# Kernel optimization log

Measured on AMD Instinct MI355X. Metric: run time of the kernel, lower is better.

The kernel has to match this reference:

```python
import jax, jax.numpy as jnp
import numpy as np

N = 50000        # num nodes
D = 128          # hidden_dim
E = 800000       # num edges (avg_degree = 16)
LN_EPS = 1e-5    # torch LayerNorm default eps


def setup_inputs() -> dict:
    key = jax.random.key(0)
    ks = jax.random.split(key, 8)
    x = jax.random.normal(ks[0], (N, D), dtype=jnp.float32)
    edge_rows = jax.random.randint(ks[1], (E,), 0, N, dtype=jnp.int32)
    edge_cols = jax.random.randint(ks[2], (E,), 0, N, dtype=jnp.int32)
    # Parameters (xavier_uniform for lin1 gain=1.0, lin2 gain=0.5; zero biases)
    lim1 = float(np.sqrt(6.0 / (D + D)))           # gain 1.0
    lim2 = 0.5 * float(np.sqrt(6.0 / (D + D)))     # gain 0.5
    W1 = jax.random.uniform(ks[3], (D, D), minval=-lim1, maxval=lim1, dtype=jnp.float32)
    W2 = jax.random.uniform(ks[4], (D, D), minval=-lim2, maxval=lim2, dtype=jnp.float32)
    b1 = jnp.zeros((D,), dtype=jnp.float32)
    b2 = jnp.zeros((D,), dtype=jnp.float32)
    gamma = jnp.ones((D,), dtype=jnp.float32)      # LayerNorm weight
    beta = jnp.zeros((D,), dtype=jnp.float32)      # LayerNorm bias
    eps = jnp.zeros((), dtype=jnp.float32)         # learnable eps, init 0.0
    return {"x": x, "edge_rows": edge_rows, "edge_cols": edge_cols,
            "W1": W1, "b1": b1, "W2": W2, "b2": b2,
            "gamma": gamma, "beta": beta, "eps": eps}


def layer_norm(x, gamma, beta):
    mu = jnp.mean(x, axis=-1, keepdims=True)
    var = jnp.mean((x - mu) ** 2, axis=-1, keepdims=True)
    return (x - mu) * jax.lax.rsqrt(var + LN_EPS) * gamma + beta


def reference(x, edge_rows, edge_cols, W1, b1, W2, b2, gamma, beta, eps):
    h = layer_norm(x, gamma, beta)                               # [N, D]
    # sparse.mm(adj_t, h): neighbor_sum[i] = sum over edges (i <- j) of h[j]
    neighbor_sum = jax.ops.segment_sum(h[edge_cols], edge_rows, num_segments=N)
    h = (1.0 + eps) * h + neighbor_sum
    h = jax.nn.silu(h @ W1.T + b1)                               # lin1 + SiLU
    h = h @ W2.T + b2                                            # lin2 (dropout p=0 -> identity)
    return x + h
```

## Files before the change

kernel.cpp:

```cpp
#include <hip/hip_runtime.h>
#include <hip/hip_bf16.h>

#define N_NODES 50000
#define DIM 128
#define N_EDGES 800000
#define NBUCKETS 196
#define BINA_EPB 4096
#define NBLKA 196
#define SEGCAP 64
#define BUCKET_CAP 6144
#define LN_BLOCKS 12500

typedef __bf16 bf16_t;
typedef bf16_t bf16x2 __attribute__((ext_vector_type(2)));
typedef bf16_t bf16x4 __attribute__((ext_vector_type(4)));
typedef bf16_t bf16x8 __attribute__((ext_vector_type(8)));
typedef float f32x4 __attribute__((ext_vector_type(4)));

__device__ __forceinline__ float bf_lo(unsigned int u) {
  return __uint_as_float(u << 16);
}
__device__ __forceinline__ float bf_hi(unsigned int u) {
  return __uint_as_float(u & 0xffff0000u);
}

__global__ __launch_bounds__(256) void k_ln_binA(
    const float* __restrict__ x, const float* __restrict__ gamma,
    const float* __restrict__ beta, bf16_t* __restrict__ h,
    const int* __restrict__ erows, const int* __restrict__ ecols,
    unsigned int* __restrict__ tmp, int* __restrict__ cnt) {
  __shared__ int sh_hist[256];
  __shared__ int sh_cur[256];
  const int t = threadIdx.x;

  if (blockIdx.x < NBLKA) {
    const int blk = blockIdx.x;
    sh_hist[t] = 0;
    __syncthreads();
    const int base = blk * BINA_EPB;
    int bkt[16];
    unsigned int pk[16];
#pragma unroll
    for (int i = 0; i < 16; ++i) {
      const int e = base + i * 256 + t;
      if (e < N_EDGES) {
        const int d = erows[e];
        bkt[i] = d >> 8;
        pk[i] = ((unsigned int)(d & 255) << 16) | (unsigned int)ecols[e];
        atomicAdd(&sh_hist[bkt[i]], 1);
      } else {
        bkt[i] = -1;
      }
    }
    __syncthreads();
    if (t < NBUCKETS) cnt[t * NBLKA + blk] = min(sh_hist[t], SEGCAP);
    sh_cur[t] = 0;
    __syncthreads();
#pragma unroll
    for (int i = 0; i < 16; ++i) {
      if (bkt[i] >= 0) {
        const int pos = atomicAdd(&sh_cur[bkt[i]], 1);
        if (pos < SEGCAP)
          tmp[((size_t)bkt[i] * NBLKA + blk) * SEGCAP + pos] = pk[i];
      }
    }
    return;
  }

  const int lane = t & 63;
  const int row  = (blockIdx.x - NBLKA) * 4 + (t >> 6);
  const float2 v = *(const float2*)(x + (size_t)row * DIM + lane * 2);
  float s  = v.x + v.y;
  float ss = v.x * v.x + v.y * v.y;
#pragma unroll
  for (int d = 1; d < 64; d <<= 1) {
    s  += __shfl_xor(s, d);
    ss += __shfl_xor(ss, d);
  }
  const float mu   = s * (1.0f / 128.0f);
  const float var  = ss * (1.0f / 128.0f) - mu * mu;
  const float rstd = rsqrtf(var + 1e-5f);
  const float2 g = *(const float2*)(gamma + lane * 2);
  const float2 b = *(const float2*)(beta + lane * 2);
  const float h0 = (v.x - mu) * rstd * g.x + b.x;
  const float h1 = (v.y - mu) * rstd * g.y + b.y;
  *(bf16x2*)(h + (size_t)row * DIM + lane * 2) = (bf16x2){(bf16_t)h0, (bf16_t)h1};
}

__global__ __launch_bounds__(256) void k_binB(
    const unsigned int* __restrict__ tmp, const int* __restrict__ cnt,
    int* __restrict__ nstart, int* __restrict__ nend,
    unsigned short* __restrict__ sorted) {
  __shared__ unsigned int stage[BUCKET_CAP];
  __shared__ int sh_cnt[256];
  __shared__ int sh_cur[256];
  __shared__ int wsum[4];
  const int b = blockIdx.x, t = threadIdx.x;
  const int lane = t & 63, w = t >> 6;

  const int c = (t < NBLKA) ? cnt[b * NBLKA + t] : 0;
  int v = c;
#pragma unroll
  for (int d = 1; d < 64; d <<= 1) {
    const int n = __shfl_up(v, d);
    if (lane >= d) v += n;
  }
  if (lane == 63) wsum[w] = v;
  __syncthreads();
  int woff = 0;
  for (int k = 0; k < w; ++k) woff += wsum[k];
  const int soff = v + woff - c;
  int total = wsum[0] + wsum[1] + wsum[2] + wsum[3];
  if (total > BUCKET_CAP) total = BUCKET_CAP;

  if (c > 0) {
    const unsigned int* seg = tmp + ((size_t)b * NBLKA + t) * SEGCAP;
    for (int j = 0; j < c; ++j) {
      const int p = soff + j;
      if (p < BUCKET_CAP) stage[p] = seg[j];
    }
  }
  __syncthreads();

  sh_cnt[t] = 0;
  __syncthreads();
  for (int e = t; e < total; e += 256)
    atomicAdd(&sh_cnt[stage[e] >> 16], 1);
  __syncthreads();

  const int val = sh_cnt[t];
  int v2 = val;
#pragma unroll
  for (int d = 1; d < 64; d <<= 1) {
    const int n = __shfl_up(v2, d);
    if (lane >= d) v2 += n;
  }
  __syncthreads();
  if (lane == 63) wsum[w] = v2;
  __syncthreads();
  int woff2 = 0;
  for (int k = 0; k < w; ++k) woff2 += wsum[k];
  const int rs = b * BUCKET_CAP;
  const int st = rs + v2 + woff2 - val;
  const int nidx = b * 256 + t;
  if (nidx < N_NODES) { nstart[nidx] = st; nend[nidx] = st + val; }
  sh_cur[t] = st;
  __syncthreads();

  for (int e = t; e < total; e += 256) {
    const unsigned int pv = stage[e];
    const int pos = atomicAdd(&sh_cur[pv >> 16], 1);
    sorted[pos] = (unsigned short)(pv & 0xffffu);
  }
}

__global__ __launch_bounds__(256) void k_gather(
    const uint2* __restrict__ h4, const int* __restrict__ nstart,
    const int* __restrict__ nend, const unsigned short* __restrict__ sorted,
    const float* __restrict__ epsp, bf16_t* __restrict__ acc) {
  const int tid  = threadIdx.x;
  const int lane = tid & 63;
  const int half = lane >> 5;
  const int l31  = lane & 31;
  const int node = blockIdx.x * 4 + (tid >> 6);
  const int s = nstart[node], e = nend[node];
  f32x4 a0 = {0.f, 0.f, 0.f, 0.f};
  f32x4 a1 = {0.f, 0.f, 0.f, 0.f};
  f32x4 a2 = {0.f, 0.f, 0.f, 0.f};
  f32x4 a3 = {0.f, 0.f, 0.f, 0.f};
  for (int base = s; base < e; base += 64) {
    const int cnt = e - base;
    const int m = cnt < 64 ? cnt : 64;
    const int myidx = (lane < m) ? (int)sorted[base + lane] : 0;
    for (int j = 0; j < m; j += 8) {
      const int o0 = j + half;
      const int o1 = j + 2 + half;
      const int o2 = j + 4 + half;
      const int o3 = j + 6 + half;
      const int s0 = __shfl(myidx, o0);
      const int s1 = __shfl(myidx, o1);
      const int s2 = __shfl(myidx, o2);
      const int s3 = __shfl(myidx, o3);
      uint2 v0 = h4[(size_t)s0 * 32 + l31];
      uint2 v1 = h4[(size_t)s1 * 32 + l31];
      uint2 v2 = h4[(size_t)s2 * 32 + l31];
      uint2 v3 = h4[(size_t)s3 * 32 + l31];
      if (o0 >= m) { v0.x = 0u; v0.y = 0u; }
      if (o1 >= m) { v1.x = 0u; v1.y = 0u; }
      if (o2 >= m) { v2.x = 0u; v2.y = 0u; }
      if (o3 >= m) { v3.x = 0u; v3.y = 0u; }
      a0[0] += bf_lo(v0.x); a0[1] += bf_hi(v0.x);
      a0[2] += bf_lo(v0.y); a0[3] += bf_hi(v0.y);
      a1[0] += bf_lo(v1.x); a1[1] += bf_hi(v1.x);
      a1[2] += bf_lo(v1.y); a1[3] += bf_hi(v1.y);
      a2[0] += bf_lo(v2.x); a2[1] += bf_hi(v2.x);
      a2[2] += bf_lo(v2.y); a2[3] += bf_hi(v2.y);
      a3[0] += bf_lo(v3.x); a3[1] += bf_hi(v3.x);
      a3[2] += bf_lo(v3.y); a3[3] += bf_hi(v3.y);
    }
  }
  f32x4 t = (a0 + a1) + (a2 + a3);
#pragma unroll
  for (int k = 0; k < 4; ++k) t[k] += __shfl_xor(t[k], 32);
  if (half == 0) {
    const uint2 hv = h4[(size_t)node * 32 + l31];
    const float epv = 1.0f + epsp[0];
    t[0] += bf_lo(hv.x) * epv; t[1] += bf_hi(hv.x) * epv;
    t[2] += bf_lo(hv.y) * epv; t[3] += bf_hi(hv.y) * epv;
    *(bf16x4*)(acc + (size_t)node * DIM + l31 * 4) =
        (bf16x4){(bf16_t)t[0], (bf16_t)t[1], (bf16_t)t[2], (bf16_t)t[3]};
  }
}

__global__ __launch_bounds__(256) void k_mlp(
    const bf16_t* __restrict__ acc, const float* __restrict__ x,
    const float* __restrict__ W1, const float* __restrict__ b1,
    const float* __restrict__ W2, const float* __restrict__ b2,
    float* __restrict__ out) {
  __shared__ __attribute__((aligned(16))) bf16_t lsA[128 * 136];
  __shared__ __attribute__((aligned(16))) bf16_t lsB[128 * 136];

  const int tid  = threadIdx.x;
  const int lane = tid & 63;
  const int w    = tid >> 6;
  const int l15  = lane & 15;
  const int lq   = lane >> 4;

#pragma unroll
  for (int i = 0; i < 16; ++i) {
    const int idx = i * 1024 + tid * 4;
    const int r = idx >> 7, c = idx & 127;
    const float4 v1 = *(const float4*)(W1 + idx);
    const float4 v2 = *(const float4*)(W2 + idx);
    *(bf16x4*)&lsA[r * 136 + c] =
        (bf16x4){(bf16_t)v1.x, (bf16_t)v1.y, (bf16_t)v1.z, (bf16_t)v1.w};
    *(bf16x4*)&lsB[r * 136 + c] =
        (bf16x4){(bf16_t)v2.x, (bf16_t)v2.y, (bf16_t)v2.z, (bf16_t)v2.w};
  }

  const int rb = blockIdx.x * 128 + w * 32;

  bf16x8 af[2][4];
#pragma unroll
  for (int t = 0; t < 2; ++t)
#pragma unroll
    for (int ks = 0; ks < 4; ++ks) {
      int row = rb + t * 16 + l15;
      row = row < N_NODES ? row : N_NODES - 1;
      af[t][ks] = *(const bf16x8*)(acc + (size_t)row * DIM + ks * 32 + lq * 8);
    }
  __syncthreads();

  f32x4 c1[2][8] = {};
#pragma unroll
  for (int cb = 0; cb < 8; ++cb)
#pragma unroll
    for (int ks = 0; ks < 4; ++ks) {
      const bf16x8 bf = *(const bf16x8*)&lsA[(cb * 16 + l15) * 136 + ks * 32 + lq * 8];
      c1[0][cb] = __builtin_amdgcn_mfma_f32_16x16x32_bf16(af[0][ks], bf, c1[0][cb], 0, 0, 0);
      c1[1][cb] = __builtin_amdgcn_mfma_f32_16x16x32_bf16(af[1][ks], bf, c1[1][cb], 0, 0, 0);
    }
  __syncthreads();

#pragma unroll
  for (int cb = 0; cb < 8; ++cb) {
    const float b1v = b1[cb * 16 + l15];
#pragma unroll
    for (int t = 0; t < 2; ++t)
#pragma unroll
      for (int r = 0; r < 4; ++r) {
        float v = c1[t][cb][r] + b1v;
        v = v / (1.0f + __expf(-v));
        const int ri = w * 32 + t * 16 + lq * 4 + r;
        lsA[ri * 136 + cb * 16 + l15] = (bf16_t)v;
      }
  }
  __syncthreads();

  bf16x8 a2[2][4];
#pragma unroll
  for (int t = 0; t < 2; ++t)
#pragma unroll
    for (int ks = 0; ks < 4; ++ks)
      a2[t][ks] = *(const bf16x8*)&lsA[(w * 32 + t * 16 + l15) * 136 + ks * 32 + lq * 8];

  f32x4 c2[2][8] = {};
#pragma unroll
  for (int cb = 0; cb < 8; ++cb)
#pragma unroll
    for (int ks = 0; ks < 4; ++ks) {
      const bf16x8 bf = *(const bf16x8*)&lsB[(cb * 16 + l15) * 136 + ks * 32 + lq * 8];
      c2[0][cb] = __builtin_amdgcn_mfma_f32_16x16x32_bf16(a2[0][ks], bf, c2[0][cb], 0, 0, 0);
      c2[1][cb] = __builtin_amdgcn_mfma_f32_16x16x32_bf16(a2[1][ks], bf, c2[1][cb], 0, 0, 0);
    }

#pragma unroll
  for (int cb = 0; cb < 8; ++cb) {
    const int c = cb * 16 + l15;
    const float b2v = b2[c];
#pragma unroll
    for (int t = 0; t < 2; ++t)
#pragma unroll
      for (int r = 0; r < 4; ++r) {
        const int row = rb + t * 16 + lq * 4 + r;
        if (row < N_NODES)
          out[(size_t)row * DIM + c] = x[(size_t)row * DIM + c] + c2[t][cb][r] + b2v;
      }
  }
}

extern "C" void kernel_launch(void* const* d_in, const int* in_sizes, int n_in,
                              void* d_out, int out_size, void* d_ws, size_t ws_size,
                              hipStream_t stream) {
  const float* x     = (const float*)d_in[0];
  const int*   erows = (const int*)d_in[1];
  const int*   ecols = (const int*)d_in[2];
  const float* W1    = (const float*)d_in[3];
  const float* b1    = (const float*)d_in[4];
  const float* W2    = (const float*)d_in[5];
  const float* b2    = (const float*)d_in[6];
  const float* gamma = (const float*)d_in[7];
  const float* beta  = (const float*)d_in[8];
  const float* eps   = (const float*)d_in[9];
  float* out = (float*)d_out;

  char* ws = (char*)d_ws;
  bf16_t* h         = (bf16_t*)(ws);
  bf16_t* acc       = (bf16_t*)(ws + 12800000);
  unsigned int* tmp = (unsigned int*)(ws + 12800000);
  unsigned short* sorted = (unsigned short*)(ws + 25600000);
  int*    nstart    = (int*)(ws + 28008448);
  int*    nend      = (int*)(ws + 28208448);
  int*    cnt       = (int*)(ws + 28408448);

  k_ln_binA<<<LN_BLOCKS + NBLKA, 256, 0, stream>>>(x, gamma, beta, h,
                                                   erows, ecols, tmp, cnt);
  k_binB  <<<NBUCKETS, 256, 0, stream>>>(tmp, cnt, nstart, nend, sorted);
  k_gather<<<N_NODES / 4, 256, 0, stream>>>((const uint2*)h, nstart, nend, sorted, eps, acc);
  k_mlp   <<<(N_NODES + 127) / 128, 256, 0, stream>>>(acc, x, W1, b1, W2, b2, out);
}
```

Before: 88.67 us.

## Fuse bucket sort and neighbor gather into one per-bucket kernel

Merges the bucket-sort kernel and the gather kernel into a single launch. Each of 196 blocks, now 1024 threads, sorts its bucket's edges into shared memory and then gathers neighbor rows for its 256 nodes. The temp bucket stride is padded to 64 KiB so that a block's acc output exactly overlays the temp region it has already consumed. This removes a kernel launch and the global round trip for sorted indices and node offsets. In exchange, the gather runs on only 196 blocks, each wave handling 16 nodes in sequence, which sharply reduces parallelism and latency hiding compared with the previous 12500-block gather.

```diff
diff --git a/kernel.cpp b/kernel.cpp
--- a/kernel.cpp
+++ b/kernel.cpp
@@ -10,6 +10,7 @@
 #define SEGCAP 64
 #define BUCKET_CAP 6144
 #define LN_BLOCKS 12500
+#define BSTRIDE_U32 16384
 
 typedef __bf16 bf16_t;
 typedef bf16_t bf16x2 __attribute__((ext_vector_type(2)));
@@ -61,7 +62,7 @@
       if (bkt[i] >= 0) {
         const int pos = atomicAdd(&sh_cur[bkt[i]], 1);
         if (pos < SEGCAP)
-          tmp[((size_t)bkt[i] * NBLKA + blk) * SEGCAP + pos] = pk[i];
+          tmp[(size_t)bkt[i] * BSTRIDE_U32 + blk * SEGCAP + pos] = pk[i];
       }
     }
     return;
@@ -87,128 +88,139 @@
   *(bf16x2*)(h + (size_t)row * DIM + lane * 2) = (bf16x2){(bf16_t)h0, (bf16_t)h1};
 }
 
-__global__ __launch_bounds__(256) void k_binB(
+__global__ __launch_bounds__(1024) void k_binB_gather(
     const unsigned int* __restrict__ tmp, const int* __restrict__ cnt,
-    int* __restrict__ nstart, int* __restrict__ nend,
-    unsigned short* __restrict__ sorted) {
+    const uint2* __restrict__ h4, const float* __restrict__ epsp,
+    bf16_t* __restrict__ acc) {
   __shared__ unsigned int stage[BUCKET_CAP];
+  __shared__ unsigned short sortedL[BUCKET_CAP];
+  __shared__ int segoff[256];
+  __shared__ int segcnt[256];
   __shared__ int sh_cnt[256];
+  __shared__ int nst[256], nen[256];
   __shared__ int sh_cur[256];
   __shared__ int wsum[4];
   const int b = blockIdx.x, t = threadIdx.x;
   const int lane = t & 63, w = t >> 6;
 
-  const int c = (t < NBLKA) ? cnt[b * NBLKA + t] : 0;
-  int v = c;
-#pragma unroll
-  for (int d = 1; d < 64; d <<= 1) {
-    const int n = __shfl_up(v, d);
-    if (lane >= d) v += n;
-  }
-  if (lane == 63) wsum[w] = v;
-  __syncthreads();
-  int woff = 0;
-  for (int k = 0; k < w; ++k) woff += wsum[k];
-  const int soff = v + woff - c;
+  int c = 0, v = 0;
+  if (t < 256) {
+    c = (t < NBLKA) ? cnt[b * NBLKA + t] : 0;
+    segcnt[t] = c;
+    v = c;
+#pragma unroll
+    for (int d = 1; d < 64; d <<= 1) {
+      const int n = __shfl_up(v, d);
+      if (lane >= d) v += n;
+    }
+    if (lane == 63) wsum[w] = v;
+  }
+  __syncthreads();
   int total = wsum[0] + wsum[1] + wsum[2] + wsum[3];
   if (total > BUCKET_CAP) total = BUCKET_CAP;
-
-  if (c > 0) {
-    const unsigned int* seg = tmp + ((size_t)b * NBLKA + t) * SEGCAP;
-    for (int j = 0; j < c; ++j) {
-      const int p = soff + j;
-      if (p < BUCKET_CAP) stage[p] = seg[j];
-    }
-  }
-  __syncthreads();
-
-  sh_cnt[t] = 0;
-  __syncthreads();
-  for (int e = t; e < total; e += 256)
+  if (t < 256) {
+    int woff = 0;
+    for (int k = 0; k < w; ++k) woff += wsum[k];
+    segoff[t] = v + woff - c;
+    sh_cnt[t] = 0;
+  }
+  __syncthreads();
+
+  {
+    const int seg = t >> 2, sub = t & 3;
+    if (seg < NBLKA) {
+      const int cs = segcnt[seg], so = segoff[seg];
+      const unsigned int* sp = tmp + (size_t)b * BSTRIDE_U32 + seg * SEGCAP;
+      for (int j = sub; j < cs; j += 4)
+        if (so + j < BUCKET_CAP) stage[so + j] = sp[j];
+    }
+  }
+  __syncthreads();
+
+  for (int e = t; e < total; e += 1024)
     atomicAdd(&sh_cnt[stage[e] >> 16], 1);
   __syncthreads();
 
-  const int val = sh_cnt[t];
-  int v2 = val;
-#pragma unroll
-  for (int d = 1; d < 64; d <<= 1) {
-    const int n = __shfl_up(v2, d);
-    if (lane >= d) v2 += n;
-  }
-  __syncthreads();
-  if (lane == 63) wsum[w] = v2;
-  __syncthreads();
-  int woff2 = 0;
-  for (int k = 0; k < w; ++k) woff2 += wsum[k];
-  const int rs = b * BUCKET_CAP;
-  const int st = rs + v2 + woff2 - val;
-  const int nidx = b * 256 + t;
-  if (nidx < N_NODES) { nstart[nidx] = st; nend[nidx] = st + val; }
-  sh_cur[t] = st;
-  __syncthreads();
-
-  for (int e = t; e < total; e += 256) {
+  int val = 0, v2 = 0;
+  if (t < 256) {
+    val = sh_cnt[t];
+    v2 = val;
+#pragma unroll
+    for (int d = 1; d < 64; d <<= 1) {
+      const int n = __shfl_up(v2, d);
+      if (lane >= d) v2 += n;
+    }
+    if (lane == 63) wsum[w] = v2;
+  }
+  __syncthreads();
+  if (t < 256) {
+    int woff = 0;
+    for (int k = 0; k < w; ++k) woff += wsum[k];
+    const int st = v2 + woff - val;
+    nst[t] = st; nen[t] = st + val;
+    sh_cur[t] = st;
+  }
+  __syncthreads();
+
+  for (int e = t; e < total; e += 1024) {
     const unsigned int pv = stage[e];
     const int pos = atomicAdd(&sh_cur[pv >> 16], 1);
-    sorted[pos] = (unsigned short)(pv & 0xffffu);
-  }
-}
-
-__global__ __launch_bounds__(256) void k_gather(
-    const uint2* __restrict__ h4, const int* __restrict__ nstart,
-    const int* __restrict__ nend, const unsigned short* __restrict__ sorted,
-    const float* __restrict__ epsp, bf16_t* __restrict__ acc) {
-  const int tid  = threadIdx.x;
-  const int lane = tid & 63;
+    sortedL[pos] = (unsigned short)(pv & 0xffffu);
+  }
+  __syncthreads();
+
   const int half = lane >> 5;
   const int l31  = lane & 31;
-  const int node = blockIdx.x * 4 + (tid >> 6);
-  const int s = nstart[node], e = nend[node];
-  f32x4 a0 = {0.f, 0.f, 0.f, 0.f};
-  f32x4 a1 = {0.f, 0.f, 0.f, 0.f};
-  f32x4 a2 = {0.f, 0.f, 0.f, 0.f};
-  f32x4 a3 = {0.f, 0.f, 0.f, 0.f};
-  for (int base = s; base < e; base += 64) {
-    const int cnt = e - base;
-    const int m = cnt < 64 ? cnt : 64;
-    const int myidx = (lane < m) ? (int)sorted[base + lane] : 0;
-    for (int j = 0; j < m; j += 8) {
-      const int o0 = j + half;
-      const int o1 = j + 2 + half;
-      const int o2 = j + 4 + half;
-      const int o3 = j + 6 + half;
-      const int s0 = __shfl(myidx, o0);
-      const int s1 = __shfl(myidx, o1);
-      const int s2 = __shfl(myidx, o2);
-      const int s3 = __shfl(myidx, o3);
-      uint2 v0 = h4[(size_t)s0 * 32 + l31];
-      uint2 v1 = h4[(size_t)s1 * 32 + l31];
-      uint2 v2 = h4[(size_t)s2 * 32 + l31];
-      uint2 v3 = h4[(size_t)s3 * 32 + l31];
-      if (o0 >= m) { v0.x = 0u; v0.y = 0u; }
-      if (o1 >= m) { v1.x = 0u; v1.y = 0u; }
-      if (o2 >= m) { v2.x = 0u; v2.y = 0u; }
-      if (o3 >= m) { v3.x = 0u; v3.y = 0u; }
-      a0[0] += bf_lo(v0.x); a0[1] += bf_hi(v0.x);
-      a0[2] += bf_lo(v0.y); a0[3] += bf_hi(v0.y);
-      a1[0] += bf_lo(v1.x); a1[1] += bf_hi(v1.x);
-      a1[2] += bf_lo(v1.y); a1[3] += bf_hi(v1.y);
-      a2[0] += bf_lo(v2.x); a2[1] += bf_hi(v2.x);
-      a2[2] += bf_lo(v2.y); a2[3] += bf_hi(v2.y);
-      a3[0] += bf_lo(v3.x); a3[1] += bf_hi(v3.x);
-      a3[2] += bf_lo(v3.y); a3[3] += bf_hi(v3.y);
-    }
-  }
-  f32x4 t = (a0 + a1) + (a2 + a3);
-#pragma unroll
-  for (int k = 0; k < 4; ++k) t[k] += __shfl_xor(t[k], 32);
-  if (half == 0) {
-    const uint2 hv = h4[(size_t)node * 32 + l31];
-    const float epv = 1.0f + epsp[0];
-    t[0] += bf_lo(hv.x) * epv; t[1] += bf_hi(hv.x) * epv;
-    t[2] += bf_lo(hv.y) * epv; t[3] += bf_hi(hv.y) * epv;
-    *(bf16x4*)(acc + (size_t)node * DIM + l31 * 4) =
-        (bf16x4){(bf16_t)t[0], (bf16_t)t[1], (bf16_t)t[2], (bf16_t)t[3]};
+  const float epv = 1.0f + epsp[0];
+  for (int n = w * 16; n < w * 16 + 16; ++n) {
+    const int gnode = b * 256 + n;
+    if (gnode >= N_NODES) continue;
+    const int s = nst[n], e = nen[n];
+    f32x4 a0 = {0.f, 0.f, 0.f, 0.f};
+    f32x4 a1 = {0.f, 0.f, 0.f, 0.f};
+    f32x4 a2 = {0.f, 0.f, 0.f, 0.f};
+    f32x4 a3 = {0.f, 0.f, 0.f, 0.f};
+    for (int base = s; base < e; base += 64) {
+      const int cnt2 = e - base;
+      const int m = cnt2 < 64 ? cnt2 : 64;
+      const int myidx = (lane < m) ? (int)sortedL[base + lane] : 0;
+      for (int j = 0; j < m; j += 8) {
+        const int o0 = j + half;
+        const int o1 = j + 2 + half;
+        const int o2 = j + 4 + half;
+        const int o3 = j + 6 + half;
+        const int s0 = __shfl(myidx, o0);
+        const int s1 = __shfl(myidx, o1);
+        const int s2 = __shfl(myidx, o2);
+        const int s3 = __shfl(myidx, o3);
+        uint2 v0 = h4[(size_t)s0 * 32 + l31];
+        uint2 v1 = h4[(size_t)s1 * 32 + l31];
+        uint2 v2_ = h4[(size_t)s2 * 32 + l31];
+        uint2 v3 = h4[(size_t)s3 * 32 + l31];
+        if (o0 >= m) { v0.x = 0u; v0.y = 0u; }
+        if (o1 >= m) { v1.x = 0u; v1.y = 0u; }
+        if (o2 >= m) { v2_.x = 0u; v2_.y = 0u; }
+        if (o3 >= m) { v3.x = 0u; v3.y = 0u; }
+        a0[0] += bf_lo(v0.x); a0[1] += bf_hi(v0.x);
+        a0[2] += bf_lo(v0.y); a0[3] += bf_hi(v0.y);
+        a1[0] += bf_lo(v1.x); a1[1] += bf_hi(v1.x);
+        a1[2] += bf_lo(v1.y); a1[3] += bf_hi(v1.y);
+        a2[0] += bf_lo(v2_.x); a2[1] += bf_hi(v2_.x);
+        a2[2] += bf_lo(v2_.y); a2[3] += bf_hi(v2_.y);
+        a3[0] += bf_lo(v3.x); a3[1] += bf_hi(v3.x);
+        a3[2] += bf_lo(v3.y); a3[3] += bf_hi(v3.y);
+      }
+    }
+    f32x4 tt = (a0 + a1) + (a2 + a3);
+#pragma unroll
+    for (int k = 0; k < 4; ++k) tt[k] += __shfl_xor(tt[k], 32);
+    if (half == 0) {
+      const uint2 hv = h4[(size_t)gnode * 32 + l31];
+      tt[0] += bf_lo(hv.x) * epv; tt[1] += bf_hi(hv.x) * epv;
+      tt[2] += bf_lo(hv.y) * epv; tt[3] += bf_hi(hv.y) * epv;
+      *(bf16x4*)(acc + (size_t)gnode * DIM + l31 * 4) =
+          (bf16x4){(bf16_t)tt[0], (bf16_t)tt[1], (bf16_t)tt[2], (bf16_t)tt[3]};
+    }
   }
 }
 
@@ -328,14 +340,10 @@
   bf16_t* h         = (bf16_t*)(ws);
   bf16_t* acc       = (bf16_t*)(ws + 12800000);
   unsigned int* tmp = (unsigned int*)(ws + 12800000);
-  unsigned short* sorted = (unsigned short*)(ws + 25600000);
-  int*    nstart    = (int*)(ws + 28008448);
-  int*    nend      = (int*)(ws + 28208448);
-  int*    cnt       = (int*)(ws + 28408448);
+  int*    cnt       = (int*)(ws + 25700000);
 
   k_ln_binA<<<LN_BLOCKS + NBLKA, 256, 0, stream>>>(x, gamma, beta, h,
                                                    erows, ecols, tmp, cnt);
-  k_binB  <<<NBUCKETS, 256, 0, stream>>>(tmp, cnt, nstart, nend, sorted);
-  k_gather<<<N_NODES / 4, 256, 0, stream>>>((const uint2*)h, nstart, nend, sorted, eps, acc);
-  k_mlp   <<<(N_NODES + 127) / 128, 256, 0, stream>>>(acc, x, W1, b1, W2, b2, out);
-}
+  k_binB_gather<<<NBUCKETS, 1024, 0, stream>>>(tmp, cnt, (const uint2*)h, eps, acc);
+  k_mlp<<<(N_NODES + 127) / 128, 256, 0, stream>>>(acc, x, W1, b1, W2, b2, out);
+}
```

After: 90.27 us. No clear change (+1.8%).

## Fuse neighbor gather into MLP kernel and pre-convert weights to bf16

Applied to the files above, without the earlier changes.

Merges the gather and MLP kernels so that each 256-thread block aggregates 16 nodes into shared memory and immediately runs both MFMA matmuls on them. This removes the bf16 acc round-trip through global memory and one kernel launch. The weights are converted to bf16 once by extra blocks in the first kernel, and each wave now reads its W rows directly from global memory (L2-resident) rather than staging full weight tiles in LDS. The risks are lower MFMA reuse per block, since each block covers only 16 rows, and serialized gather latency of 4 nodes per wave before the matmul. The tmp layout stride also changes so tmp no longer overlaps acc.

```diff
diff --git a/kernel.cpp b/kernel.cpp
--- a/kernel.cpp
+++ b/kernel.cpp
@@ -8,6 +8,7 @@
 #define BINA_EPB 4096
 #define NBLKA 196
 #define SEGCAP 64
+#define BSTRIDE_U32 16384
 #define BUCKET_CAP 6144
 #define LN_BLOCKS 12500
 
@@ -28,7 +29,9 @@
     const float* __restrict__ x, const float* __restrict__ gamma,
     const float* __restrict__ beta, bf16_t* __restrict__ h,
     const int* __restrict__ erows, const int* __restrict__ ecols,
-    unsigned int* __restrict__ tmp, int* __restrict__ cnt) {
+    unsigned int* __restrict__ tmp, int* __restrict__ cnt,
+    const float* __restrict__ W1, const float* __restrict__ W2,
+    bf16_t* __restrict__ W1b, bf16_t* __restrict__ W2b) {
   __shared__ int sh_hist[256];
   __shared__ int sh_cur[256];
   const int t = threadIdx.x;
@@ -61,14 +64,28 @@
       if (bkt[i] >= 0) {
         const int pos = atomicAdd(&sh_cur[bkt[i]], 1);
         if (pos < SEGCAP)
-          tmp[((size_t)bkt[i] * NBLKA + blk) * SEGCAP + pos] = pk[i];
+          tmp[(size_t)bkt[i] * BSTRIDE_U32 + blk * SEGCAP + pos] = pk[i];
       }
     }
     return;
   }
 
+  if (blockIdx.x < NBLKA + 8) {
+    const int wid = blockIdx.x - NBLKA;
+    const float* src = (wid < 4) ? W1 : W2;
+    bf16_t* dst = (wid < 4) ? W1b : W2b;
+    const int off = (wid & 3) * 4096 + t * 16;
+#pragma unroll
+    for (int k = 0; k < 16; k += 4) {
+      const float4 u = *(const float4*)(src + off + k);
+      *(bf16x4*)(dst + off + k) =
+          (bf16x4){(bf16_t)u.x, (bf16_t)u.y, (bf16_t)u.z, (bf16_t)u.w};
+    }
+    return;
+  }
+
   const int lane = t & 63;
-  const int row  = (blockIdx.x - NBLKA) * 4 + (t >> 6);
+  const int row  = (blockIdx.x - NBLKA - 8) * 4 + (t >> 6);
   const float2 v = *(const float2*)(x + (size_t)row * DIM + lane * 2);
   float s  = v.x + v.y;
   float ss = v.x * v.x + v.y * v.y;
@@ -114,7 +131,7 @@
   if (total > BUCKET_CAP) total = BUCKET_CAP;
 
   if (c > 0) {
-    const unsigned int* seg = tmp + ((size_t)b * NBLKA + t) * SEGCAP;
+    const unsigned int* seg = tmp + (size_t)b * BSTRIDE_U32 + t * SEGCAP;
     for (int j = 0; j < c; ++j) {
       const int p = soff + j;
       if (p < BUCKET_CAP) stage[p] = seg[j];
@@ -154,158 +171,131 @@
   }
 }
 
-__global__ __launch_bounds__(256) void k_gather(
+__global__ __launch_bounds__(256) void k_gm(
     const uint2* __restrict__ h4, const int* __restrict__ nstart,
     const int* __restrict__ nend, const unsigned short* __restrict__ sorted,
-    const float* __restrict__ epsp, bf16_t* __restrict__ acc) {
-  const int tid  = threadIdx.x;
-  const int lane = tid & 63;
-  const int half = lane >> 5;
-  const int l31  = lane & 31;
-  const int node = blockIdx.x * 4 + (tid >> 6);
-  const int s = nstart[node], e = nend[node];
-  f32x4 a0 = {0.f, 0.f, 0.f, 0.f};
-  f32x4 a1 = {0.f, 0.f, 0.f, 0.f};
-  f32x4 a2 = {0.f, 0.f, 0.f, 0.f};
-  f32x4 a3 = {0.f, 0.f, 0.f, 0.f};
-  for (int base = s; base < e; base += 64) {
-    const int cnt = e - base;
-    const int m = cnt < 64 ? cnt : 64;
-    const int myidx = (lane < m) ? (int)sorted[base + lane] : 0;
-    for (int j = 0; j < m; j += 8) {
-      const int o0 = j + half;
-      const int o1 = j + 2 + half;
-      const int o2 = j + 4 + half;
-      const int o3 = j + 6 + half;
-      const int s0 = __shfl(myidx, o0);
-      const int s1 = __shfl(myidx, o1);
-      const int s2 = __shfl(myidx, o2);
-      const int s3 = __shfl(myidx, o3);
-      uint2 v0 = h4[(size_t)s0 * 32 + l31];
-      uint2 v1 = h4[(size_t)s1 * 32 + l31];
-      uint2 v2 = h4[(size_t)s2 * 32 + l31];
-      uint2 v3 = h4[(size_t)s3 * 32 + l31];
-      if (o0 >= m) { v0.x = 0u; v0.y = 0u; }
-      if (o1 >= m) { v1.x = 0u; v1.y = 0u; }
-      if (o2 >= m) { v2.x = 0u; v2.y = 0u; }
-      if (o3 >= m) { v3.x = 0u; v3.y = 0u; }
-      a0[0] += bf_lo(v0.x); a0[1] += bf_hi(v0.x);
-      a0[2] += bf_lo(v0.y); a0[3] += bf_hi(v0.y);
-      a1[0] += bf_lo(v1.x); a1[1] += bf_hi(v1.x);
-      a1[2] += bf_lo(v1.y); a1[3] += bf_hi(v1.y);
-      a2[0] += bf_lo(v2.x); a2[1] += bf_hi(v2.x);
-      a2[2] += bf_lo(v2.y); a2[3] += bf_hi(v2.y);
-      a3[0] += bf_lo(v3.x); a3[1] += bf_hi(v3.x);
-      a3[2] += bf_lo(v3.y); a3[3] += bf_hi(v3.y);
-    }
-  }
-  f32x4 t = (a0 + a1) + (a2 + a3);
-#pragma unroll
-  for (int k = 0; k < 4; ++k) t[k] += __shfl_xor(t[k], 32);
-  if (half == 0) {
-    const uint2 hv = h4[(size_t)node * 32 + l31];
-    const float epv = 1.0f + epsp[0];
-    t[0] += bf_lo(hv.x) * epv; t[1] += bf_hi(hv.x) * epv;
-    t[2] += bf_lo(hv.y) * epv; t[3] += bf_hi(hv.y) * epv;
-    *(bf16x4*)(acc + (size_t)node * DIM + l31 * 4) =
-        (bf16x4){(bf16_t)t[0], (bf16_t)t[1], (bf16_t)t[2], (bf16_t)t[3]};
-  }
-}
-
-__global__ __launch_bounds__(256) void k_mlp(
-    const bf16_t* __restrict__ acc, const float* __restrict__ x,
-    const float* __restrict__ W1, const float* __restrict__ b1,
-    const float* __restrict__ W2, const float* __restrict__ b2,
+    const float* __restrict__ epsp, const float* __restrict__ x,
+    const bf16_t* __restrict__ W1b, const float* __restrict__ b1,
+    const bf16_t* __restrict__ W2b, const float* __restrict__ b2,
     float* __restrict__ out) {
-  __shared__ __attribute__((aligned(16))) bf16_t lsA[128 * 136];
-  __shared__ __attribute__((aligned(16))) bf16_t lsB[128 * 136];
-
-  const int tid  = threadIdx.x;
-  const int lane = tid & 63;
-  const int w    = tid >> 6;
-  const int l15  = lane & 15;
-  const int lq   = lane >> 4;
-
-#pragma unroll
-  for (int i = 0; i < 16; ++i) {
-    const int idx = i * 1024 + tid * 4;
-    const int r = idx >> 7, c = idx & 127;
-    const float4 v1 = *(const float4*)(W1 + idx);
-    const float4 v2 = *(const float4*)(W2 + idx);
-    *(bf16x4*)&lsA[r * 136 + c] =
-        (bf16x4){(bf16_t)v1.x, (bf16_t)v1.y, (bf16_t)v1.z, (bf16_t)v1.w};
-    *(bf16x4*)&lsB[r * 136 + c] =
-        (bf16x4){(bf16_t)v2.x, (bf16_t)v2.y, (bf16_t)v2.z, (bf16_t)v2.w};
-  }
-
-  const int rb = blockIdx.x * 128 + w * 32;
-
-  bf16x8 af[2][4];
-#pragma unroll
-  for (int t = 0; t < 2; ++t)
+  __shared__ __attribute__((aligned(16))) bf16_t accL[16 * 136];
+  __shared__ __attribute__((aligned(16))) bf16_t interL[16 * 136];
+  const int t = threadIdx.x, lane = t & 63, w = t >> 6;
+  const int half = lane >> 5, l31 = lane & 31;
+  const int nodebase = blockIdx.x * 16;
+  const float epv = 1.0f + epsp[0];
+
+  for (int i = 0; i < 4; ++i) {
+    const int n = w * 4 + i;
+    const int gnode = nodebase + n;
+    const int s = nstart[gnode], e = nend[gnode];
+    f32x4 a0 = {0.f, 0.f, 0.f, 0.f};
+    f32x4 a1 = {0.f, 0.f, 0.f, 0.f};
+    f32x4 a2v = {0.f, 0.f, 0.f, 0.f};
+    f32x4 a3 = {0.f, 0.f, 0.f, 0.f};
+    for (int base = s; base < e; base += 64) {
+      const int cnt2 = e - base;
+      const int m = cnt2 < 64 ? cnt2 : 64;
+      const int myidx = (lane < m) ? (int)sorted[base + lane] : 0;
+      for (int j = 0; j < m; j += 8) {
+        const int o0 = j + half;
+        const int o1 = j + 2 + half;
+        const int o2 = j + 4 + half;
+        const int o3 = j + 6 + half;
+        const int s0 = __shfl(myidx, o0);
+        const int s1 = __shfl(myidx, o1);
+        const int s2 = __shfl(myidx, o2);
+        const int s3 = __shfl(myidx, o3);
+        uint2 v0 = h4[(size_t)s0 * 32 + l31];
+        uint2 v1 = h4[(size_t)s1 * 32 + l31];
+        uint2 v2 = h4[(size_t)s2 * 32 + l31];
+        uint2 v3 = h4[(size_t)s3 * 32 + l31];
+        if (o0 >= m) { v0.x = 0u; v0.y = 0u; }
+        if (o1 >= m) { v1.x = 0u; v1.y = 0u; }
+        if (o2 >= m) { v2.x = 0u; v2.y = 0u; }
+        if (o3 >= m) { v3.x = 0u; v3.y = 0u; }
+        a0[0] += bf_lo(v0.x); a0[1] += bf_hi(v0.x);
+        a0[2] += bf_lo(v0.y); a0[3] += bf_hi(v0.y);
+        a1[0] += bf_lo(v1.x); a1[1] += bf_hi(v1.x);
+        a1[2] += bf_lo(v1.y); a1[3] += bf_hi(v1.y);
+        a2v[0] += bf_lo(v2.x); a2v[1] += bf_hi(v2.x);
+        a2v[2] += bf_lo(v2.y); a2v[3] += bf_hi(v2.y);
+        a3[0] += bf_lo(v3.x); a3[1] += bf_hi(v3.x);
+        a3[2] += bf_lo(v3.y); a3[3] += bf_hi(v3.y);
+      }
+    }
+    f32x4 tt = (a0 + a1) + (a2v + a3);
+#pragma unroll
+    for (int k = 0; k < 4; ++k) tt[k] += __shfl_xor(tt[k], 32);
+    if (half == 0) {
+      const uint2 hv = h4[(size_t)gnode * 32 + l31];
+      tt[0] += bf_lo(hv.x) * epv; tt[1] += bf_hi(hv.x) * epv;
+      tt[2] += bf_lo(hv.y) * epv; tt[3] += bf_hi(hv.y) * epv;
+      *(bf16x4*)&accL[n * 136 + l31 * 4] =
+          (bf16x4){(bf16_t)tt[0], (bf16_t)tt[1], (bf16_t)tt[2], (bf16_t)tt[3]};
+    }
+  }
+  __syncthreads();
+
+  const int l15 = lane & 15, lq = lane >> 4;
+
+  bf16x8 af[4];
+#pragma unroll
+  for (int ks = 0; ks < 4; ++ks)
+    af[ks] = *(const bf16x8*)&accL[l15 * 136 + ks * 32 + lq * 8];
+
+  f32x4 c1[2] = {};
+#pragma unroll
+  for (int cbh = 0; cbh < 2; ++cbh) {
+    const int cb = w * 2 + cbh;
+    const bf16_t* wrow = W1b + (size_t)(cb * 16 + l15) * DIM;
 #pragma unroll
     for (int ks = 0; ks < 4; ++ks) {
-      int row = rb + t * 16 + l15;
-      row = row < N_NODES ? row : N_NODES - 1;
-      af[t][ks] = *(const bf16x8*)(acc + (size_t)row * DIM + ks * 32 + lq * 8);
-    }
-  __syncthreads();
-
-  f32x4 c1[2][8] = {};
-#pragma unroll
-  for (int cb = 0; cb < 8; ++cb)
+      const bf16x8 bf = *(const bf16x8*)(wrow + ks * 32 + lq * 8);
+      c1[cbh] = __builtin_amdgcn_mfma_f32_16x16x32_bf16(af[ks], bf, c1[cbh], 0, 0, 0);
+    }
+  }
+
+#pragma unroll
+  for (int cbh = 0; cbh < 2; ++cbh) {
+    const int cb = w * 2 + cbh;
+    const float b1v = b1[cb * 16 + l15];
+#pragma unroll
+    for (int r = 0; r < 4; ++r) {
+      float v = c1[cbh][r] + b1v;
+      v = v / (1.0f + __expf(-v));
+      interL[(lq * 4 + r) * 136 + cb * 16 + l15] = (bf16_t)v;
+    }
+  }
+  __syncthreads();
+
+  bf16x8 a2[4];
+#pragma unroll
+  for (int ks = 0; ks < 4; ++ks)
+    a2[ks] = *(const bf16x8*)&interL[l15 * 136 + ks * 32 + lq * 8];
+
+  f32x4 c2[2] = {};
+#pragma unroll
+  for (int cbh = 0; cbh < 2; ++cbh) {
+    const int cb = w * 2 + cbh;
+    const bf16_t* wrow = W2b + (size_t)(cb * 16 + l15) * DIM;
 #pragma unroll
     for (int ks = 0; ks < 4; ++ks) {
-      const bf16x8 bf = *(const bf16x8*)&lsA[(cb * 16 + l15) * 136 + ks * 32 + lq * 8];
-      c1[0][cb] = __builtin_amdgcn_mfma_f32_16x16x32_bf16(af[0][ks], bf, c1[0][cb], 0, 0, 0);
-      c1[1][cb] = __builtin_amdgcn_mfma_f32_16x16x32_bf16(af[1][ks], bf, c1[1][cb], 0, 0, 0);
-    }
-  __syncthreads();
-
-#pragma unroll
-  for (int cb = 0; cb < 8; ++cb) {
-    const float b1v = b1[cb * 16 + l15];
-#pragma unroll
-    for (int t = 0; t < 2; ++t)
-#pragma unroll
-      for (int r = 0; r < 4; ++r) {
-        float v = c1[t][cb][r] + b1v;
-        v = v / (1.0f + __expf(-v));
-        const int ri = w * 32 + t * 16 + lq * 4 + r;
-        lsA[ri * 136 + cb * 16 + l15] = (bf16_t)v;
-      }
-  }
-  __syncthreads();
-
-  bf16x8 a2[2][4];
-#pragma unroll
-  for (int t = 0; t < 2; ++t)
-#pragma unroll
-    for (int ks = 0; ks < 4; ++ks)
-      a2[t][ks] = *(const bf16x8*)&lsA[(w * 32 + t * 16 + l15) * 136 + ks * 32 + lq * 8];
-
-  f32x4 c2[2][8] = {};
-#pragma unroll
-  for (int cb = 0; cb < 8; ++cb)
-#pragma unroll
-    for (int ks = 0; ks < 4; ++ks) {
-      const bf16x8 bf = *(const bf16x8*)&lsB[(cb * 16 + l15) * 136 + ks * 32 + lq * 8];
-      c2[0][cb] = __builtin_amdgcn_mfma_f32_16x16x32_bf16(a2[0][ks], bf, c2[0][cb], 0, 0, 0);
-      c2[1][cb] = __builtin_amdgcn_mfma_f32_16x16x32_bf16(a2[1][ks], bf, c2[1][cb], 0, 0, 0);
-    }
-
-#pragma unroll
-  for (int cb = 0; cb < 8; ++cb) {
+      const bf16x8 bf = *(const bf16x8*)(wrow + ks * 32 + lq * 8);
+      c2[cbh] = __builtin_amdgcn_mfma_f32_16x16x32_bf16(a2[ks], bf, c2[cbh], 0, 0, 0);
+    }
+  }
+
+#pragma unroll
+  for (int cbh = 0; cbh < 2; ++cbh) {
+    const int cb = w * 2 + cbh;
     const int c = cb * 16 + l15;
     const float b2v = b2[c];
 #pragma unroll
-    for (int t = 0; t < 2; ++t)
-#pragma unroll
-      for (int r = 0; r < 4; ++r) {
-        const int row = rb + t * 16 + lq * 4 + r;
-        if (row < N_NODES)
-          out[(size_t)row * DIM + c] = x[(size_t)row * DIM + c] + c2[t][cb][r] + b2v;
-      }
+    for (int r = 0; r < 4; ++r) {
+      const size_t row = nodebase + lq * 4 + r;
+      out[row * DIM + c] = x[row * DIM + c] + c2[cbh][r] + b2v;
+    }
   }
 }
 
@@ -326,16 +316,17 @@
 
   char* ws = (char*)d_ws;
   bf16_t* h         = (bf16_t*)(ws);
-  bf16_t* acc       = (bf16_t*)(ws + 12800000);
   unsigned int* tmp = (unsigned int*)(ws + 12800000);
-  unsigned short* sorted = (unsigned short*)(ws + 25600000);
-  int*    nstart    = (int*)(ws + 28008448);
-  int*    nend      = (int*)(ws + 28208448);
-  int*    cnt       = (int*)(ws + 28408448);
-
-  k_ln_binA<<<LN_BLOCKS + NBLKA, 256, 0, stream>>>(x, gamma, beta, h,
-                                                   erows, ecols, tmp, cnt);
-  k_binB  <<<NBUCKETS, 256, 0, stream>>>(tmp, cnt, nstart, nend, sorted);
-  k_gather<<<N_NODES / 4, 256, 0, stream>>>((const uint2*)h, nstart, nend, sorted, eps, acc);
-  k_mlp   <<<(N_NODES + 127) / 128, 256, 0, stream>>>(acc, x, W1, b1, W2, b2, out);
-}
+  int*    cnt       = (int*)(ws + 25645056);
+  unsigned short* sorted = (unsigned short*)(ws + 25798720);
+  int*    nstart    = (int*)(ws + 28207168);
+  int*    nend      = (int*)(ws + 28407168);
+  bf16_t* W1b       = (bf16_t*)(ws + 28607168);
+  bf16_t* W2b       = (bf16_t*)(ws + 28639936);
+
+  k_ln_binA<<<NBLKA + 8 + LN_BLOCKS, 256, 0, stream>>>(
+      x, gamma, beta, h, erows, ecols, tmp, cnt, W1, W2, W1b, W2b);
+  k_binB<<<NBUCKETS, 256, 0, stream>>>(tmp, cnt, nstart, nend, sorted);
+  k_gm<<<N_NODES / 16, 256, 0, stream>>>(
+      (const uint2*)h, nstart, nend, sorted, eps, x, W1b, b1, W2b, b2, out);
+}
```

Result: faster. 82.77 us (median of 2 runs) (-6.7%).
